# Kernel tuning notes

Hardware: AMD Instinct MI355X
Metric: run time of the kernel (lower is better)

## Reference

```python
import jax, jax.numpy as jnp
import numpy as np

N_NODES = 100000
N_EDGES = 1600000
F_IN, HID, N_CLS = 512, 256, 40


def setup_inputs() -> dict:
    key = jax.random.key(0)
    k1, k2, k3, k4 = jax.random.split(key, 4)
    features = jax.random.normal(k1, (N_NODES, F_IN), dtype=jnp.float32)
    # Glorot-ish scaled weights
    W1 = jax.random.normal(k2, (F_IN, HID), dtype=jnp.float32) * (1.0 / np.sqrt(F_IN))
    b1 = jnp.zeros((HID,), dtype=jnp.float32)
    W2 = jax.random.normal(k3, (HID, N_CLS), dtype=jnp.float32) * (1.0 / np.sqrt(HID))
    b2 = jnp.zeros((N_CLS,), dtype=jnp.float32)
    edge_index = jax.random.randint(k4, (2, N_EDGES), 0, N_NODES, dtype=jnp.int64)
    return {"features": features, "W1": W1, "b1": b1, "W2": W2, "b2": b2,
            "edge_index": edge_index}


def _gcn_conv(x, W, b, src, dst, n_nodes):
    # PyG GCNConv: h = X W; out = D^{-1/2}(A+I)D^{-1/2} h + b
    h = x @ W  # [N, out]
    # degree with self-loops (in-degree on dst + 1)
    deg = jax.ops.segment_sum(jnp.ones_like(dst, dtype=h.dtype), dst,
                              num_segments=n_nodes) + 1.0
    dinv = jax.lax.rsqrt(deg)  # [N]
    norm = dinv[src] * dinv[dst]  # [E]
    # gather-normalize-scatter over edges, plus self-loop term dinv_i^2 * h_i
    agg = jax.ops.segment_sum(h[src] * norm[:, None], dst, num_segments=n_nodes)
    agg = agg + h * (dinv * dinv)[:, None]
    return agg + b


def reference(features, W1, b1, W2, b2, edge_index):
    src, dst = edge_index[0], edge_index[1]
    n = features.shape[0]
    x = jax.nn.relu(_gcn_conv(features, W1, b1, src, dst, n))
    # dropout is identity in eval mode (training=False)
    x = _gcn_conv(x, W2, b2, src, dst, n)
    return jax.nn.log_softmax(x, axis=1), jax.nn.softmax(x, axis=1)
```

## Files before the change

kernel.cpp:

```cpp
#include <hip/hip_runtime.h>
#include <hip/hip_bf16.h>


#define F_IN 512
#define HID  256
#define NCLS 40
#define NPAD 48

typedef __attribute__((ext_vector_type(8))) short bf16x8;
typedef __attribute__((ext_vector_type(4))) float floatx4;

__device__ inline unsigned short f2bf(float v) {
    unsigned u = __float_as_uint(v);
    u += 0x7fffu + ((u >> 16) & 1u);
    return (unsigned short)(u >> 16);
}
__device__ inline float bf2f(unsigned short u) {
    return __uint_as_float(((unsigned)u) << 16);
}

__global__ void detect64_kernel(const int* __restrict__ ei, int* __restrict__ flag) {
    __shared__ int any_nz;
    if (threadIdx.x == 0) any_nz = 0;
    __syncthreads();
    int nz = 0;
    for (int i = threadIdx.x; i < 4096; i += 256) {
        nz |= (ei[2 * i + 1] != 0);
    }
    if (nz) atomicOr(&any_nz, 1);
    __syncthreads();
    if (threadIdx.x == 0) *flag = any_nz ? 0 : 1;
}

__device__ inline int edge_src(const int* ei, long long E, int e, int is64) {
    return is64 ? ei[2LL * e] : ei[e];
}
__device__ inline int edge_dst(const int* ei, long long E, int e, int is64) {
    return is64 ? ei[2LL * (E + e)] : ei[(int)E + e];
}

__global__ void count_kernel(const int* __restrict__ ei, int E,
                             const int* __restrict__ flag, int* __restrict__ cnt) {
    int e = blockIdx.x * 256 + threadIdx.x;
    if (e >= E) return;
    int is64 = *flag;
    int d = edge_dst(ei, E, e, is64);
    atomicAdd(&cnt[d], 1);
}

__global__ __launch_bounds__(256) void scan_block_sums(const int* __restrict__ cnt,
                                                       int* __restrict__ blockSums, int Nn) {
    __shared__ int sdata[256];
    int b = blockIdx.x, t = threadIdx.x;
    int sum = 0;
    int i0 = b * 1024 + t * 4;
    for (int i = 0; i < 4; ++i) {
        int idx = i0 + i;
        if (idx < Nn) sum += cnt[idx];
    }
    sdata[t] = sum;
    __syncthreads();
    for (int s = 128; s > 0; s >>= 1) {
        if (t < s) sdata[t] += sdata[t + s];
        __syncthreads();
    }
    if (t == 0) blockSums[b] = sdata[0];
}

__global__ void scan_sums_kernel(int* __restrict__ blockSums, int nB,
                                 int* __restrict__ rowStart, int Nn) {
    if (threadIdx.x == 0 && blockIdx.x == 0) {
        int run = 0;
        for (int i = 0; i < nB; ++i) { int v = blockSums[i]; blockSums[i] = run; run += v; }
        rowStart[Nn] = run;
    }
}

__global__ __launch_bounds__(256) void scan_final(const int* __restrict__ cnt,
                                                  const int* __restrict__ blockSumsEx,
                                                  int* __restrict__ rowStart,
                                                  int* __restrict__ rowPos, int Nn) {
    __shared__ int sdata[256];
    int b = blockIdx.x, t = threadIdx.x;
    int base = blockSumsEx[b];
    int vals[4];
    int sum = 0;
    int i0 = b * 1024 + t * 4;
    for (int i = 0; i < 4; ++i) {
        int idx = i0 + i;
        vals[i] = (idx < Nn) ? cnt[idx] : 0;
        sum += vals[i];
    }
    sdata[t] = sum;
    __syncthreads();
    for (int off = 1; off < 256; off <<= 1) {
        int y = (t >= off) ? sdata[t - off] : 0;
        __syncthreads();
        sdata[t] += y;
        __syncthreads();
    }
    int run = base + (sdata[t] - sum);
    for (int i = 0; i < 4; ++i) {
        int idx = i0 + i;
        if (idx < Nn) { rowStart[idx] = run; rowPos[idx] = run; }
        run += vals[i];
    }
}

__global__ void dinv_kernel(const int* __restrict__ cnt, float* __restrict__ dinv, int Nn) {
    int i = blockIdx.x * 256 + threadIdx.x;
    if (i < Nn) dinv[i] = rsqrtf((float)cnt[i] + 1.0f);
}

__global__ void fill_kernel(const int* __restrict__ ei, int E, const int* __restrict__ flag,
                            const float* __restrict__ dinv, int* __restrict__ rowPos,
                            int* __restrict__ csrSrc, float* __restrict__ csrNorm) {
    int e = blockIdx.x * 256 + threadIdx.x;
    if (e >= E) return;
    int is64 = *flag;
    int s = edge_src(ei, E, e, is64);
    int d = edge_dst(ei, E, e, is64);
    int p = atomicAdd(&rowPos[d], 1);
    csrSrc[p] = s;
    csrNorm[p] = dinv[s] * dinv[d];
}

__global__ __launch_bounds__(256) void convertW1t_kernel(const float* __restrict__ W1,
                                                         unsigned short* __restrict__ W1t) {
    int id = blockIdx.x * 256 + threadIdx.x;
    int k = id >> 8, n = id & 255;
    W1t[n * 512 + k] = f2bf(W1[id]);
}

__global__ __launch_bounds__(256) void convertW2t_kernel(const float* __restrict__ W2,
                                                         unsigned short* __restrict__ W2t) {
    int id = blockIdx.x * 256 + threadIdx.x;
    if (id >= NPAD * HID) return;
    int n = id / HID, k = id % HID;
    W2t[id] = (n < NCLS) ? f2bf(W2[k * NCLS + n]) : (unsigned short)0;
}

#define LDK 40
__global__ __launch_bounds__(256) void gemm1_mfma_kernel(const float* __restrict__ X,
                                                         const unsigned short* __restrict__ W1t,
                                                         unsigned short* __restrict__ h1, int Nn) {
    __shared__ unsigned short As[128][LDK];
    __shared__ unsigned short Bs[128][LDK];
    const int tid = threadIdx.x;
    const int bm = blockIdx.x * 128;
    const int bn = blockIdx.y * 128;
    const int lane = tid & 63, w = tid >> 6;
    const int mblk = (w & 1) * 64, nblk = (w >> 1) * 64;
    const int lrow = lane & 15, lq = lane >> 4;

    int aRow[4], aKb[4], bRow[2], bKb[2];
#pragma unroll
    for (int i = 0; i < 4; ++i) {
        int c = tid + i * 256;
        aRow[i] = c >> 3; aKb[i] = (c & 7) * 4;
    }
#pragma unroll
    for (int i = 0; i < 2; ++i) {
        int c = tid + i * 256;
        bRow[i] = c >> 2; bKb[i] = (c & 3) * 8;
    }

    float4 aReg[2][4];
    float4 bReg[2][2];
#pragma unroll
    for (int p = 0; p < 2; ++p) {
        int kb = p * 32;
#pragma unroll
        for (int i = 0; i < 4; ++i) {
            int gm = bm + aRow[i];
            aReg[p][i] = make_float4(0.f, 0.f, 0.f, 0.f);
            if (gm < Nn) aReg[p][i] = *(const float4*)&X[(size_t)gm * F_IN + kb + aKb[i]];
        }
#pragma unroll
        for (int i = 0; i < 2; ++i)
            bReg[p][i] = *(const float4*)&W1t[(size_t)(bn + bRow[i]) * F_IN + kb + bKb[i]];
    }

    floatx4 acc[4][4];
#pragma unroll
    for (int i = 0; i < 4; ++i)
#pragma unroll
        for (int j = 0; j < 4; ++j)
            acc[i][j] = (floatx4){0.f, 0.f, 0.f, 0.f};

#pragma unroll 2
    for (int t = 0; t < F_IN / 32; ++t) {
        const int sel = t & 1;
        __syncthreads();
#pragma unroll
        for (int i = 0; i < 4; ++i) {
            ushort4 o;
            o.x = f2bf(aReg[sel][i].x); o.y = f2bf(aReg[sel][i].y);
            o.z = f2bf(aReg[sel][i].z); o.w = f2bf(aReg[sel][i].w);
            *(ushort4*)&As[aRow[i]][aKb[i]] = o;
        }
#pragma unroll
        for (int i = 0; i < 2; ++i)
            *(float4*)&Bs[bRow[i]][bKb[i]] = bReg[sel][i];
        __syncthreads();

        int kf = (t + 2) * 32;
        if (kf < F_IN) {
#pragma unroll
            for (int i = 0; i < 4; ++i) {
                int gm = bm + aRow[i];
                aReg[sel][i] = make_float4(0.f, 0.f, 0.f, 0.f);
                if (gm < Nn) aReg[sel][i] = *(const float4*)&X[(size_t)gm * F_IN + kf + aKb[i]];
            }
#pragma unroll
            for (int i = 0; i < 2; ++i)
                bReg[sel][i] = *(const float4*)&W1t[(size_t)(bn + bRow[i]) * F_IN + kf + bKb[i]];
        }

        bf16x8 a[4], b[4];
#pragma unroll
        for (int mt = 0; mt < 4; ++mt)
            a[mt] = *(const bf16x8*)&As[mblk + mt * 16 + lrow][lq * 8];
#pragma unroll
        for (int nt = 0; nt < 4; ++nt)
            b[nt] = *(const bf16x8*)&Bs[nblk + nt * 16 + lrow][lq * 8];
#pragma unroll
        for (int mt = 0; mt < 4; ++mt)
#pragma unroll
            for (int nt = 0; nt < 4; ++nt)
                acc[mt][nt] = __builtin_amdgcn_mfma_f32_16x16x32_bf16(
                    b[nt], a[mt], acc[mt][nt], 0, 0, 0);
    }
#pragma unroll
    for (int mt = 0; mt < 4; ++mt) {
        size_t gm = (size_t)(bm + mblk + mt * 16 + lrow);
#pragma unroll
        for (int nt = 0; nt < 4; ++nt) {
            int gn = bn + nblk + nt * 16 + lq * 4;
            ushort4 o;
            o.x = f2bf(acc[mt][nt][0]); o.y = f2bf(acc[mt][nt][1]);
            o.z = f2bf(acc[mt][nt][2]); o.w = f2bf(acc[mt][nt][3]);
            *(ushort4*)&h1[gm * HID + gn] = o;
        }
    }
}

__global__ __launch_bounds__(256) void agg1_kernel(const unsigned short* __restrict__ h1,
                                                   const int* __restrict__ rowStart,
                                                   const int* __restrict__ csrSrc,
                                                   const float* __restrict__ csrNorm,
                                                   const float* __restrict__ dinv,
                                                   const float* __restrict__ b1,
                                                   unsigned short* __restrict__ x1b, int Nn) {
    int n = blockIdx.x * 4 + (threadIdx.x >> 6);
    int lane = threadIdx.x & 63;
    if (n >= Nn) return;
    float4 acc = make_float4(0.f, 0.f, 0.f, 0.f);
    int s0 = rowStart[n], s1 = rowStart[n + 1];
    int e = s0;
    for (; e + 3 < s1; e += 4) {
        int iA = csrSrc[e], iB = csrSrc[e + 1], iC = csrSrc[e + 2], iD = csrSrc[e + 3];
        float nA = csrNorm[e], nB = csrNorm[e + 1], nC = csrNorm[e + 2], nD = csrNorm[e + 3];
        ushort4 vA = *(const ushort4*)(h1 + (size_t)iA * HID + lane * 4);
        ushort4 vB = *(const ushort4*)(h1 + (size_t)iB * HID + lane * 4);
        ushort4 vC = *(const ushort4*)(h1 + (size_t)iC * HID + lane * 4);
        ushort4 vD = *(const ushort4*)(h1 + (size_t)iD * HID + lane * 4);
        acc.x += nA * bf2f(vA.x) + nB * bf2f(vB.x) + nC * bf2f(vC.x) + nD * bf2f(vD.x);
        acc.y += nA * bf2f(vA.y) + nB * bf2f(vB.y) + nC * bf2f(vC.y) + nD * bf2f(vD.y);
        acc.z += nA * bf2f(vA.z) + nB * bf2f(vB.z) + nC * bf2f(vC.z) + nD * bf2f(vD.z);
        acc.w += nA * bf2f(vA.w) + nB * bf2f(vB.w) + nC * bf2f(vC.w) + nD * bf2f(vD.w);
    }
    for (; e < s1; ++e) {
        int s = csrSrc[e];
        float nrm = csrNorm[e];
        ushort4 v = *(const ushort4*)(h1 + (size_t)s * HID + lane * 4);
        acc.x += nrm * bf2f(v.x);
        acc.y += nrm * bf2f(v.y);
        acc.z += nrm * bf2f(v.z);
        acc.w += nrm * bf2f(v.w);
    }
    float di = dinv[n];
    float self = di * di;
    ushort4 hv = *(const ushort4*)(h1 + (size_t)n * HID + lane * 4);
    float4 bv = *(const float4*)(b1 + lane * 4);
    ushort4 o;
    o.x = f2bf(fmaxf(acc.x + self * bf2f(hv.x) + bv.x, 0.f));
    o.y = f2bf(fmaxf(acc.y + self * bf2f(hv.y) + bv.y, 0.f));
    o.z = f2bf(fmaxf(acc.z + self * bf2f(hv.z) + bv.z, 0.f));
    o.w = f2bf(fmaxf(acc.w + self * bf2f(hv.w) + bv.w, 0.f));
    *(ushort4*)(x1b + (size_t)n * HID + lane * 4) = o;
}

__global__ __launch_bounds__(256) void gemm2_mfma_kernel(const unsigned short* __restrict__ x1b,
                                                         const unsigned short* __restrict__ W2t,
                                                         unsigned short* __restrict__ h2b) {
    const int tid = threadIdx.x;
    const int lane = tid & 63, w = tid >> 6;
    const int base = blockIdx.x * 128 + w * 32;
    const int lrow = lane & 15, lq = lane >> 4;

    floatx4 acc[2][3];
#pragma unroll
    for (int i = 0; i < 2; ++i)
#pragma unroll
        for (int j = 0; j < 3; ++j)
            acc[i][j] = (floatx4){0.f, 0.f, 0.f, 0.f};

#pragma unroll
    for (int k0 = 0; k0 < HID; k0 += 32) {
        bf16x8 a[2], b[3];
#pragma unroll
        for (int mt = 0; mt < 2; ++mt)
            a[mt] = *(const bf16x8*)&x1b[(size_t)(base + mt * 16 + lrow) * HID + k0 + lq * 8];
#pragma unroll
        for (int nt = 0; nt < 3; ++nt)
            b[nt] = *(const bf16x8*)&W2t[(size_t)(nt * 16 + lrow) * HID + k0 + lq * 8];
#pragma unroll
        for (int mt = 0; mt < 2; ++mt)
#pragma unroll
            for (int nt = 0; nt < 3; ++nt)
                acc[mt][nt] = __builtin_amdgcn_mfma_f32_16x16x32_bf16(
                    b[nt], a[mt], acc[mt][nt], 0, 0, 0);
    }
#pragma unroll
    for (int mt = 0; mt < 2; ++mt) {
        size_t gm = (size_t)(base + mt * 16 + lrow);
#pragma unroll
        for (int nt = 0; nt < 3; ++nt) {
            int gn = nt * 16 + lq * 4;
            ushort4 o;
            o.x = f2bf(acc[mt][nt][0]); o.y = f2bf(acc[mt][nt][1]);
            o.z = f2bf(acc[mt][nt][2]); o.w = f2bf(acc[mt][nt][3]);
            *(ushort4*)&h2b[gm * NPAD + gn] = o;
        }
    }
}

__global__ __launch_bounds__(256) void agg2_kernel(const unsigned short* __restrict__ h2b,
                                                   const int* __restrict__ rowStart,
                                                   const int* __restrict__ csrSrc,
                                                   const float* __restrict__ csrNorm,
                                                   const float* __restrict__ dinv,
                                                   const float* __restrict__ b2,
                                                   float* __restrict__ out, int Nn) {
    int n = blockIdx.x * 4 + (threadIdx.x >> 6);
    int lane = threadIdx.x & 63;
    if (n >= Nn) return;
    bool act = lane < NCLS;
    int cl = act ? lane : 0;
    float acc = 0.f;
    int s0 = rowStart[n], s1 = rowStart[n + 1];
    int e = s0;
    for (; e + 3 < s1; e += 4) {
        int iA = csrSrc[e], iB = csrSrc[e + 1], iC = csrSrc[e + 2], iD = csrSrc[e + 3];
        float nA = csrNorm[e], nB = csrNorm[e + 1], nC = csrNorm[e + 2], nD = csrNorm[e + 3];
        float vA = bf2f(h2b[(size_t)iA * NPAD + cl]);
        float vB = bf2f(h2b[(size_t)iB * NPAD + cl]);
        float vC = bf2f(h2b[(size_t)iC * NPAD + cl]);
        float vD = bf2f(h2b[(size_t)iD * NPAD + cl]);
        acc += nA * vA + nB * vB + nC * vC + nD * vD;
    }
    for (; e < s1; ++e) {
        int s = csrSrc[e];
        acc += csrNorm[e] * bf2f(h2b[(size_t)s * NPAD + cl]);
    }
    float di = dinv[n];
    acc += di * di * bf2f(h2b[(size_t)n * NPAD + cl]) + b2[cl];
    float v = act ? acc : -3.4e38f;
#pragma unroll
    for (int off = 32; off > 0; off >>= 1) v = fmaxf(v, __shfl_xor(v, off));
    float ex = act ? expf(acc - v) : 0.f;
    float ssum = ex;
#pragma unroll
    for (int off = 32; off > 0; off >>= 1) ssum += __shfl_xor(ssum, off);
    if (act) {
        float ls = acc - v - logf(ssum);
        out[(size_t)n * NCLS + lane] = ls;
        out[(size_t)Nn * NCLS + (size_t)n * NCLS + lane] = ex / ssum;
    }
}

extern "C" void kernel_launch(void* const* d_in, const int* in_sizes, int n_in,
                              void* d_out, int out_size, void* d_ws, size_t ws_size,
                              hipStream_t stream) {
    const float* features = (const float*)d_in[0];
    const float* W1 = (const float*)d_in[1];
    const float* b1 = (const float*)d_in[2];
    const float* W2 = (const float*)d_in[3];
    const float* b2 = (const float*)d_in[4];
    const int* edge_index = (const int*)d_in[5];

    const int N = in_sizes[0] / F_IN;
    const int E = in_sizes[5] / 2;
    const int Mpad = (N + 127) & ~127;
    float* out = (float*)d_out;

    auto align256 = [](size_t x) { return (x + 255) & ~(size_t)255; };
    char* w = (char*)d_ws;
    int* cnt        = (int*)w;  w += align256((size_t)N * 4);
    int* rowStart   = (int*)w;  w += align256((size_t)(N + 1) * 4);
    int* rowPos     = (int*)w;  w += align256((size_t)N * 4);
    int* blockSums  = (int*)w;  w += align256(1024 * 4);
    int* flag64     = (int*)w;  w += 256;
    int* csrSrc     = (int*)w;  w += align256((size_t)E * 4);
    float* csrNorm  = (float*)w; w += align256((size_t)E * 4);
    float* dinv     = (float*)w; w += align256((size_t)N * 4);
    unsigned short* W1t = (unsigned short*)w; w += align256((size_t)HID * F_IN * 2);
    unsigned short* W2t = (unsigned short*)w; w += align256((size_t)NPAD * HID * 2);
    unsigned short* h1  = (unsigned short*)w; w += align256((size_t)Mpad * HID * 2);
    unsigned short* x1b = (unsigned short*)w; w += align256((size_t)Mpad * HID * 2);
    unsigned short* h2b = (unsigned short*)w; w += align256((size_t)Mpad * NPAD * 2);
    (void)ws_size;

    const int nB = (N + 1023) / 1024;
    const int eBlocks = (E + 255) / 256;
    const int nBlocks = (N + 255) / 256;
    const int waveBlocks = (N + 3) / 4;

    hipMemsetAsync(cnt, 0, (size_t)N * 4, stream);
    detect64_kernel<<<1, 256, 0, stream>>>(edge_index, flag64);
    count_kernel<<<eBlocks, 256, 0, stream>>>(edge_index, E, flag64, cnt);
    scan_block_sums<<<nB, 256, 0, stream>>>(cnt, blockSums, N);
    scan_sums_kernel<<<1, 64, 0, stream>>>(blockSums, nB, rowStart, N);
    dinv_kernel<<<nBlocks, 256, 0, stream>>>(cnt, dinv, N);
    scan_final<<<nB, 256, 0, stream>>>(cnt, blockSums, rowStart, rowPos, N);
    fill_kernel<<<eBlocks, 256, 0, stream>>>(edge_index, E, flag64, dinv, rowPos,
                                             csrSrc, csrNorm);

    convertW1t_kernel<<<(F_IN * HID) / 256, 256, 0, stream>>>(W1, W1t);
    convertW2t_kernel<<<(NPAD * HID + 255) / 256, 256, 0, stream>>>(W2, W2t);

    dim3 g1(Mpad / 128, HID / 128);
    gemm1_mfma_kernel<<<g1, 256, 0, stream>>>(features, W1t, h1, N);
    agg1_kernel<<<waveBlocks, 256, 0, stream>>>(h1, rowStart, csrSrc, csrNorm, dinv,
                                                b1, x1b, N);
    gemm2_mfma_kernel<<<Mpad / 128, 256, 0, stream>>>(x1b, W2t, h2b);
    agg2_kernel<<<waveBlocks, 256, 0, stream>>>(h2b, rowStart, csrSrc, csrNorm, dinv,
                                                b2, out, N);
}
```

Baseline: 781.6 us.

## Load GEMM1 tiles directly into LDS with global_load_lds and XOR swizzle

Rewrites the first GEMM's tile loading so global_load_lds copies X (fp32) and W1t straight into LDS, using an XOR-swizzled layout to avoid bank conflicts. BK grows to 64. X is now converted to bf16 at LDS-read time rather than at store time. This drops the register double-buffering and prefetch, so loads are no longer overlapped with MFMA and each tile waits on synchronous barriers. LDS use roughly doubles (fp32 A tile), which may lower occupancy.

```diff
diff --git a/kernel.cpp b/kernel.cpp
--- a/kernel.cpp
+++ b/kernel.cpp
@@ -17,6 +17,21 @@
 }
 __device__ inline float bf2f(unsigned short u) {
     return __uint_as_float(((unsigned)u) << 16);
+}
+
+__device__ inline void gload_lds16(const void* g, void* l) {
+    __builtin_amdgcn_global_load_lds(
+        (const __attribute__((address_space(1))) unsigned int*)g,
+        (__attribute__((address_space(3))) unsigned int*)l, 16, 0, 0);
+}
+
+__device__ inline bf16x8 pack8(float4 f0, float4 f1) {
+    bf16x8 r;
+    r[0] = (short)f2bf(f0.x); r[1] = (short)f2bf(f0.y);
+    r[2] = (short)f2bf(f0.z); r[3] = (short)f2bf(f0.w);
+    r[4] = (short)f2bf(f1.x); r[5] = (short)f2bf(f1.y);
+    r[6] = (short)f2bf(f1.z); r[7] = (short)f2bf(f1.w);
+    return r;
 }
 
 __global__ void detect64_kernel(const int* __restrict__ ei, int* __restrict__ flag) {
@@ -140,45 +155,31 @@
     W2t[id] = (n < NCLS) ? f2bf(W2[k * NCLS + n]) : (unsigned short)0;
 }
 
-#define LDK 40
+#define BK 64
 __global__ __launch_bounds__(256) void gemm1_mfma_kernel(const float* __restrict__ X,
                                                          const unsigned short* __restrict__ W1t,
                                                          unsigned short* __restrict__ h1, int Nn) {
-    __shared__ unsigned short As[128][LDK];
-    __shared__ unsigned short Bs[128][LDK];
+    __shared__ float As[128 * 64];
+    __shared__ unsigned short Bs[128 * 64];
     const int tid = threadIdx.x;
     const int bm = blockIdx.x * 128;
     const int bn = blockIdx.y * 128;
     const int lane = tid & 63, w = tid >> 6;
-    const int mblk = (w & 1) * 64, nblk = (w >> 1) * 64;
+    const int wr = (w & 1) * 64, wc = (w >> 1) * 64;
     const int lrow = lane & 15, lq = lane >> 4;
 
-    int aRow[4], aKb[4], bRow[2], bKb[2];
+    int aRow[8], aK[8], bRow[4], bK[4];
+#pragma unroll
+    for (int i = 0; i < 8; ++i) {
+        int c = i * 256 + w * 64 + lane;
+        int row = c >> 4, pslot = c & 15;
+        aRow[i] = row; aK[i] = (pslot ^ (row & 15)) * 4;
+    }
 #pragma unroll
     for (int i = 0; i < 4; ++i) {
-        int c = tid + i * 256;
-        aRow[i] = c >> 3; aKb[i] = (c & 7) * 4;
-    }
-#pragma unroll
-    for (int i = 0; i < 2; ++i) {
-        int c = tid + i * 256;
-        bRow[i] = c >> 2; bKb[i] = (c & 3) * 8;
-    }
-
-    float4 aReg[2][4];
-    float4 bReg[2][2];
-#pragma unroll
-    for (int p = 0; p < 2; ++p) {
-        int kb = p * 32;
-#pragma unroll
-        for (int i = 0; i < 4; ++i) {
-            int gm = bm + aRow[i];
-            aReg[p][i] = make_float4(0.f, 0.f, 0.f, 0.f);
-            if (gm < Nn) aReg[p][i] = *(const float4*)&X[(size_t)gm * F_IN + kb + aKb[i]];
-        }
-#pragma unroll
-        for (int i = 0; i < 2; ++i)
-            bReg[p][i] = *(const float4*)&W1t[(size_t)(bn + bRow[i]) * F_IN + kb + bKb[i]];
+        int c = i * 256 + w * 64 + lane;
+        int row = c >> 3, pslot = c & 7;
+        bRow[i] = row; bK[i] = (pslot ^ (row & 7)) * 8;
     }
 
     floatx4 acc[4][4];
@@ -188,55 +189,55 @@
         for (int j = 0; j < 4; ++j)
             acc[i][j] = (floatx4){0.f, 0.f, 0.f, 0.f};
 
-#pragma unroll 2
-    for (int t = 0; t < F_IN / 32; ++t) {
-        const int sel = t & 1;
+    for (int t = 0; t < F_IN / BK; ++t) {
+        const int k0 = t * BK;
         __syncthreads();
 #pragma unroll
-        for (int i = 0; i < 4; ++i) {
-            ushort4 o;
-            o.x = f2bf(aReg[sel][i].x); o.y = f2bf(aReg[sel][i].y);
-            o.z = f2bf(aReg[sel][i].z); o.w = f2bf(aReg[sel][i].w);
-            *(ushort4*)&As[aRow[i]][aKb[i]] = o;
+        for (int i = 0; i < 8; ++i) {
+            int srow = bm + aRow[i];
+            if (srow >= Nn) srow = Nn - 1;
+            gload_lds16(&X[(size_t)srow * F_IN + k0 + aK[i]],
+                        &As[(i * 256 + w * 64) * 4]);
         }
 #pragma unroll
-        for (int i = 0; i < 2; ++i)
-            *(float4*)&Bs[bRow[i]][bKb[i]] = bReg[sel][i];
+        for (int i = 0; i < 4; ++i)
+            gload_lds16(&W1t[(size_t)(bn + bRow[i]) * F_IN + k0 + bK[i]],
+                        &Bs[(i * 256 + w * 64) * 8]);
         __syncthreads();
 
-        int kf = (t + 2) * 32;
-        if (kf < F_IN) {
-#pragma unroll
-            for (int i = 0; i < 4; ++i) {
-                int gm = bm + aRow[i];
-                aReg[sel][i] = make_float4(0.f, 0.f, 0.f, 0.f);
-                if (gm < Nn) aReg[sel][i] = *(const float4*)&X[(size_t)gm * F_IN + kf + aKb[i]];
+#pragma unroll
+        for (int kh = 0; kh < 2; ++kh) {
+            bf16x8 av[4], bv[4];
+#pragma unroll
+            for (int mt = 0; mt < 4; ++mt) {
+                int row = wr + mt * 16 + lrow;
+                int m = row & 15;
+                int s0 = kh * 8 + lq * 2;
+                float4 f0 = *(const float4*)&As[row * 64 + ((s0 ^ m) << 2)];
+                float4 f1 = *(const float4*)&As[row * 64 + (((s0 + 1) ^ m) << 2)];
+                av[mt] = pack8(f0, f1);
             }
 #pragma unroll
-            for (int i = 0; i < 2; ++i)
-                bReg[sel][i] = *(const float4*)&W1t[(size_t)(bn + bRow[i]) * F_IN + kf + bKb[i]];
+            for (int nt = 0; nt < 4; ++nt) {
+                int row = wc + nt * 16 + lrow;
+                int ls = kh * 4 + lq;
+                bv[nt] = *(const bf16x8*)&Bs[row * 64 + ((ls ^ (row & 7)) << 3)];
+            }
+#pragma unroll
+            for (int mt = 0; mt < 4; ++mt)
+#pragma unroll
+                for (int nt = 0; nt < 4; ++nt)
+                    acc[mt][nt] = __builtin_amdgcn_mfma_f32_16x16x32_bf16(
+                        bv[nt], av[mt], acc[mt][nt], 0, 0, 0);
         }
-
-        bf16x8 a[4], b[4];
-#pragma unroll
-        for (int mt = 0; mt < 4; ++mt)
-            a[mt] = *(const bf16x8*)&As[mblk + mt * 16 + lrow][lq * 8];
-#pragma unroll
-        for (int nt = 0; nt < 4; ++nt)
-            b[nt] = *(const bf16x8*)&Bs[nblk + nt * 16 + lrow][lq * 8];
-#pragma unroll
-        for (int mt = 0; mt < 4; ++mt)
-#pragma unroll
-            for (int nt = 0; nt < 4; ++nt)
-                acc[mt][nt] = __builtin_amdgcn_mfma_f32_16x16x32_bf16(
-                    b[nt], a[mt], acc[mt][nt], 0, 0, 0);
-    }
+    }
+
 #pragma unroll
     for (int mt = 0; mt < 4; ++mt) {
-        size_t gm = (size_t)(bm + mblk + mt * 16 + lrow);
+        size_t gm = (size_t)(bm + wr + mt * 16 + lrow);
 #pragma unroll
         for (int nt = 0; nt < 4; ++nt) {
-            int gn = bn + nblk + nt * 16 + lq * 4;
+            int gn = bn + wc + nt * 16 + lq * 4;
             ushort4 o;
             o.x = f2bf(acc[mt][nt][0]); o.y = f2bf(acc[mt][nt][1]);
             o.z = f2bf(acc[mt][nt][2]); o.w = f2bf(acc[mt][nt][3]);
```

Result: faster. 744.9 us (-4.7%).
